# Kernel optimization log

Hardware: AMD Instinct MI355X
Metric: run time of the kernel (lower is better)

The kernel has to match this reference:

```python
import jax, jax.numpy as jnp
import numpy as np

N, IN, OUT, FAN = 4096, 4096, 4096, 64


def setup_inputs() -> dict:
    key = jax.random.key(0)
    k1, k2, k3, k4 = jax.random.split(key, 4)
    return {
        "input": jax.random.normal(k1, (N, IN), dtype=jnp.float32),
        "condensed_weight": jax.random.normal(k2, (OUT, FAN), dtype=jnp.float32) * np.float32(1.0 / np.sqrt(FAN)),
        "input_mask": jax.random.randint(k3, (OUT, FAN), 0, IN, dtype=jnp.int32),
        "bias": jax.random.normal(k4, (OUT,), dtype=jnp.float32),
    }


def reference(input, condensed_weight, input_mask, bias):
    # Fixed-fan-in sparse linear: out[b, o] = sum_k input[b, mask[o, k]] * W[o, k] + bias[o]
    # Scan over the (small, fixed) fan-in axis to avoid materializing the
    # [N, OUT, FAN] gathered tensor; each step gathers an [N, OUT] slab.
    n = input.shape[0]

    def body(acc, wk_mk):
        w_k, m_k = wk_mk            # each [OUT]
        g = jnp.take(input, m_k, axis=1)  # [N, OUT] gather of input columns
        return acc + g * w_k[None, :], None

    acc0 = jnp.zeros((n, bias.shape[0]), dtype=input.dtype) + bias[None, :]
    out, _ = jax.lax.scan(body, acc0, (condensed_weight.T, input_mask.T))
    return out
```

## Files before the change

### kernel.cpp

```cpp
#include <hip/hip_runtime.h>

#define IN_DIM   4096
#define OUT_DIM  4096
#define FAN_IN   64
#define ROWS     8
#define NTHREADS 512
#define O_PER_THREAD (OUT_DIM / NTHREADS)
#define MT_BYTES ((size_t)(FAN_IN / 4) * OUT_DIM * 16)

typedef __fp16 v2h __attribute__((ext_vector_type(2)));

__device__ __forceinline__ int bswz(int m) {
    return (m & ~7) | ((m ^ (m >> 3)) & 7);
}

__device__ __forceinline__ unsigned int pack_f16(float a, float b) {
    v2h h = __builtin_amdgcn_cvt_pkrtz(a, b);
    unsigned int u;
    __builtin_memcpy(&u, &h, sizeof(u));
    return u;
}

__global__ __launch_bounds__(256)
void transpose_mw(const int* __restrict__ M, const float* __restrict__ W,
                  int4* __restrict__ Mt, float4* __restrict__ Wt)
{
    const int t  = blockIdx.x * 256 + threadIdx.x;
    const int kk = t >> 12;
    const int o  = t & (OUT_DIM - 1);
    int4 m = ((const int4*)(M + (size_t)o * FAN_IN))[kk];
    m.x = bswz(m.x) << 4; m.y = bswz(m.y) << 4;
    m.z = bswz(m.z) << 4; m.w = bswz(m.w) << 4;
    Mt[kk * OUT_DIM + o] = m;
    Wt[kk * OUT_DIM + o] = ((const float4*)(W + (size_t)o * FAN_IN))[kk];
}

#define FMAMIX_LO(acc, pk, w)                                                  \
    asm("v_fma_mix_f32 %0, %1, %2, %0 op_sel:[0,0,0] op_sel_hi:[1,0,0]"        \
        : "+v"(acc) : "v"(pk), "v"(w))
#define FMAMIX_HI(acc, pk, w)                                                  \
    asm("v_fma_mix_f32 %0, %1, %2, %0 op_sel:[1,0,0] op_sel_hi:[1,0,0]"        \
        : "+v"(acc) : "v"(pk), "v"(w))

template <bool TRANSPOSED>
__global__ __launch_bounds__(NTHREADS, 4)
void ffi_sparse_kernel(const float* __restrict__ inp,
                       const float* __restrict__ W,
                       const int*   __restrict__ M,
                       const float* __restrict__ bias,
                       const int4*  __restrict__ Mt,
                       const float4* __restrict__ Wt,
                       float* __restrict__ out)
{
    __shared__ unsigned int lds[IN_DIM * ROWS / 2];

    const int tid = threadIdx.x;
    const int r0  = blockIdx.x * ROWS;

    #pragma unroll
    for (int t = 0; t < (ROWS * IN_DIM / 16) / NTHREADS; ++t) {
        const int tile = tid + t * NTHREADS;
        const int rblk = tile >> 10;
        const int c4   = (tile & 1023) << 2;
        const float* src = inp + (size_t)(r0 + rblk * 4) * IN_DIM + c4;
        const float4 v0 = *(const float4*)(src);
        const float4 v1 = *(const float4*)(src + IN_DIM);
        const float4 v2 = *(const float4*)(src + 2 * IN_DIM);
        const float4 v3 = *(const float4*)(src + 3 * IN_DIM);

        unsigned int* p;
        p = lds + bswz(c4 + 0) * 4 + rblk * 2;
        *(uint2*)p = make_uint2(pack_f16(v0.x, v1.x), pack_f16(v2.x, v3.x));
        p = lds + bswz(c4 + 1) * 4 + rblk * 2;
        *(uint2*)p = make_uint2(pack_f16(v0.y, v1.y), pack_f16(v2.y, v3.y));
        p = lds + bswz(c4 + 2) * 4 + rblk * 2;
        *(uint2*)p = make_uint2(pack_f16(v0.z, v1.z), pack_f16(v2.z, v3.z));
        p = lds + bswz(c4 + 3) * 4 + rblk * 2;
        *(uint2*)p = make_uint2(pack_f16(v0.w, v1.w), pack_f16(v2.w, v3.w));
    }
    __syncthreads();

    const char* __restrict__ ldsb = (const char*)lds;

#define LDQ(off) (*(const uint4*)(ldsb + (off)))

#define CONSUME(d, wv) {                                                       \
        FMAMIX_LO(acc0, d.x, wv);  FMAMIX_HI(acc1, d.x, wv);                   \
        FMAMIX_LO(acc2, d.y, wv);  FMAMIX_HI(acc3, d.y, wv);                   \
        FMAMIX_LO(acc4, d.z, wv);  FMAMIX_HI(acc5, d.z, wv);                   \
        FMAMIX_LO(acc6, d.w, wv);  FMAMIX_HI(acc7, d.w, wv);                   \
    }
#define ISSUE4(D0,D1,D2,D3, MN) {                                              \
        D0 = LDQ(MN.x); D1 = LDQ(MN.y); D2 = LDQ(MN.z); D3 = LDQ(MN.w); }
#define CONS4(D0,D1,D2,D3, WC) {                                               \
        CONSUME(D0, WC.x); CONSUME(D1, WC.y);                                  \
        CONSUME(D2, WC.z); CONSUME(D3, WC.w); }
#define MWLD(dm, dw, idx) {                                                    \
        if (TRANSPOSED) {                                                      \
            dm = Mt[(idx) * OUT_DIM + o];                                      \
            dw = Wt[(idx) * OUT_DIM + o];                                      \
        } else {                                                               \
            int4 mr = mp[(idx)];                                               \
            mr.x = bswz(mr.x) << 4; mr.y = bswz(mr.y) << 4;                    \
            mr.z = bswz(mr.z) << 4; mr.w = bswz(mr.w) << 4;                    \
            dm = mr; dw = wp[(idx)];                                           \
        } }

    #pragma unroll 1
    for (int i = 0; i < O_PER_THREAD; ++i) {
        const int o = tid + i * NTHREADS;
        const float bv = bias[o];
        float acc0 = bv, acc1 = bv, acc2 = bv, acc3 = bv;
        float acc4 = bv, acc5 = bv, acc6 = bv, acc7 = bv;

        const int4*   mp = (const int4*)(M + (size_t)o * FAN_IN);
        const float4* wp = (const float4*)(W + (size_t)o * FAN_IN);

        int4   m0, m1, m2, m3;
        float4 w0, w1, w2, w3;
        uint4  dA0, dA1, dA2, dA3, dB0, dB1, dB2, dB3;

        MWLD(m0, w0, 0);  MWLD(m1, w1, 1);  MWLD(m2, w2, 2);
        ISSUE4(dA0,dA1,dA2,dA3, m0);

        ISSUE4(dB0,dB1,dB2,dB3, m1);  MWLD(m3,w3, 3);   CONS4(dA0,dA1,dA2,dA3, w0);
        ISSUE4(dA0,dA1,dA2,dA3, m2);  MWLD(m0,w0, 4);   CONS4(dB0,dB1,dB2,dB3, w1);
        ISSUE4(dB0,dB1,dB2,dB3, m3);  MWLD(m1,w1, 5);   CONS4(dA0,dA1,dA2,dA3, w2);
        ISSUE4(dA0,dA1,dA2,dA3, m0);  MWLD(m2,w2, 6);   CONS4(dB0,dB1,dB2,dB3, w3);
        ISSUE4(dB0,dB1,dB2,dB3, m1);  MWLD(m3,w3, 7);   CONS4(dA0,dA1,dA2,dA3, w0);
        ISSUE4(dA0,dA1,dA2,dA3, m2);  MWLD(m0,w0, 8);   CONS4(dB0,dB1,dB2,dB3, w1);
        ISSUE4(dB0,dB1,dB2,dB3, m3);  MWLD(m1,w1, 9);   CONS4(dA0,dA1,dA2,dA3, w2);
        ISSUE4(dA0,dA1,dA2,dA3, m0);  MWLD(m2,w2,10);   CONS4(dB0,dB1,dB2,dB3, w3);
        ISSUE4(dB0,dB1,dB2,dB3, m1);  MWLD(m3,w3,11);   CONS4(dA0,dA1,dA2,dA3, w0);
        ISSUE4(dA0,dA1,dA2,dA3, m2);  MWLD(m0,w0,12);   CONS4(dB0,dB1,dB2,dB3, w1);
        ISSUE4(dB0,dB1,dB2,dB3, m3);  MWLD(m1,w1,13);   CONS4(dA0,dA1,dA2,dA3, w2);
        ISSUE4(dA0,dA1,dA2,dA3, m0);  MWLD(m2,w2,14);   CONS4(dB0,dB1,dB2,dB3, w3);
        ISSUE4(dB0,dB1,dB2,dB3, m1);  MWLD(m3,w3,15);   CONS4(dA0,dA1,dA2,dA3, w0);
        ISSUE4(dA0,dA1,dA2,dA3, m2);                    CONS4(dB0,dB1,dB2,dB3, w1);
        ISSUE4(dB0,dB1,dB2,dB3, m3);                    CONS4(dA0,dA1,dA2,dA3, w2);
                                                        CONS4(dB0,dB1,dB2,dB3, w3);

        float* op = out + (size_t)r0 * OUT_DIM + o;
        op[0 * OUT_DIM] = acc0;
        op[1 * OUT_DIM] = acc1;
        op[2 * OUT_DIM] = acc2;
        op[3 * OUT_DIM] = acc3;
        op[4 * OUT_DIM] = acc4;
        op[5 * OUT_DIM] = acc5;
        op[6 * OUT_DIM] = acc6;
        op[7 * OUT_DIM] = acc7;
    }
#undef CONSUME
#undef ISSUE4
#undef CONS4
#undef MWLD
#undef LDQ
}

extern "C" void kernel_launch(void* const* d_in, const int* in_sizes, int n_in,
                              void* d_out, int out_size, void* d_ws, size_t ws_size,
                              hipStream_t stream) {
    const float* inp  = (const float*)d_in[0];
    const float* W    = (const float*)d_in[1];
    const int*   M    = (const int*)d_in[2];
    const float* bias = (const float*)d_in[3];
    float* out = (float*)d_out;

    const int n_rows = in_sizes[0] / IN_DIM;
    dim3 grid(n_rows / ROWS), block(NTHREADS);

    const bool use_t = ws_size >= 2 * MT_BYTES;
    if (use_t) {
        int4*   Mt = (int4*)d_ws;
        float4* Wt = (float4*)((char*)d_ws + MT_BYTES);
        transpose_mw<<<dim3(OUT_DIM * (FAN_IN / 4) / 256), dim3(256), 0, stream>>>(M, W, Mt, Wt);
        ffi_sparse_kernel<true><<<grid, block, 0, stream>>>(inp, W, M, bias, Mt, Wt, out);
    } else {
        ffi_sparse_kernel<false><<<grid, block, 0, stream>>>(inp, W, M, bias,
                                                             (const int4*)nullptr,
                                                             (const float4*)nullptr, out);
    }
}
```

Before: 74.55 us.

## Reorder fan-in indices per output to spread LDS bank groups across lanes

The preprocessing kernel now handles one output per thread and reorders its 64 fan-in entries by LDS bank group. Each step s aims for group (s+o)&7, so neighbouring lanes read different bank groups at the same time, which is meant to cut LDS bank conflicts in the gather loop. The cost is that the setup kernel becomes serial per thread with large local arrays, likely spilling to scratch, and it launches only 16 blocks. That extra setup time adds to the total.

Result: slower. 133.1 us (+78.5%).

```diff
diff --git a/kernel.cpp b/kernel.cpp
--- a/kernel.cpp
+++ b/kernel.cpp
@@ -22,17 +22,47 @@
 }
 
 __global__ __launch_bounds__(256)
-void transpose_mw(const int* __restrict__ M, const float* __restrict__ W,
-                  int4* __restrict__ Mt, float4* __restrict__ Wt)
+void schedule_mw(const int* __restrict__ M, const float* __restrict__ W,
+                 int4* __restrict__ Mt, float4* __restrict__ Wt)
 {
-    const int t  = blockIdx.x * 256 + threadIdx.x;
-    const int kk = t >> 12;
-    const int o  = t & (OUT_DIM - 1);
-    int4 m = ((const int4*)(M + (size_t)o * FAN_IN))[kk];
-    m.x = bswz(m.x) << 4; m.y = bswz(m.y) << 4;
-    m.z = bswz(m.z) << 4; m.w = bswz(m.w) << 4;
-    Mt[kk * OUT_DIM + o] = m;
-    Wt[kk * OUT_DIM + o] = ((const float4*)(W + (size_t)o * FAN_IN))[kk];
+    const int o = blockIdx.x * 256 + threadIdx.x;
+
+    int   mm[FAN_IN];
+    float ww[FAN_IN];
+    int   gg[FAN_IN];
+    for (int k = 0; k < FAN_IN; ++k) {
+        const int m = M[(size_t)o * FAN_IN + k];
+        mm[k] = bswz(m) << 4;
+        gg[k] = (mm[k] >> 4) & 7;
+        ww[k] = W[(size_t)o * FAN_IN + k];
+    }
+    int cnt[8] = {0,0,0,0,0,0,0,0};
+    for (int k = 0; k < FAN_IN; ++k) cnt[gg[k]]++;
+    int start[8]; int acc0 = 0;
+    for (int g = 0; g < 8; ++g) { start[g] = acc0; acc0 += cnt[g]; }
+    int fill[8] = {0,0,0,0,0,0,0,0};
+    int order[FAN_IN];
+    for (int k = 0; k < FAN_IN; ++k) order[start[gg[k]] + fill[gg[k]]++] = k;
+    int ptr[8] = {0,0,0,0,0,0,0,0};
+    int4 tm; float4 tw;
+    for (int s = 0; s < FAN_IN; ++s) {
+        int d = (s + o) & 7;
+        if (ptr[d] >= cnt[d]) {
+            int best = 0, bestrem = -1;
+            for (int g = 0; g < 8; ++g) {
+                const int rem = cnt[g] - ptr[g];
+                if (rem > bestrem) { bestrem = rem; best = g; }
+            }
+            d = best;
+        }
+        const int k = order[start[d] + ptr[d]++];
+        ((int*)&tm)[s & 3]   = mm[k];
+        ((float*)&tw)[s & 3] = ww[k];
+        if ((s & 3) == 3) {
+            Mt[(s >> 2) * OUT_DIM + o] = tm;
+            Wt[(s >> 2) * OUT_DIM + o] = tw;
+        }
+    }
 }
 
 #define FMAMIX_LO(acc, pk, w)                                                  \
@@ -173,7 +203,7 @@
     if (use_t) {
         int4*   Mt = (int4*)d_ws;
         float4* Wt = (float4*)((char*)d_ws + MT_BYTES);
-        transpose_mw<<<dim3(OUT_DIM * (FAN_IN / 4) / 256), dim3(256), 0, stream>>>(M, W, Mt, Wt);
+        schedule_mw<<<dim3(OUT_DIM / 256), dim3(256), 0, stream>>>(M, W, Mt, Wt);
         ffi_sparse_kernel<true><<<grid, block, 0, stream>>>(inp, W, M, bias, Mt, Wt, out);
     } else {
         ffi_sparse_kernel<false><<<grid, block, 0, stream>>>(inp, W, M, bias,
```

## Reorder per-output fan-in indices to spread LDS gathers across banks

Applied to the files above, without the earlier changes.

The preprocessing kernel now permutes each output's 64 (index, weight) pairs instead of only transposing them. Each pair is assigned to a slot by its LDS bank group and rotated by the output index, so the 16-byte gathers issued together by neighbouring threads fall into different bank groups. Overflow entries from crowded groups fill the gaps left by sparse ones. This targets LDS bank conflicts in the main gather-FMA loop, at the cost of a more complex ballot/popcount scheduling pass, and it relies on the sum being order-independent.

Measured after the change: 71.99 us. 3.4% less time.

```diff
diff --git a/kernel.cpp b/kernel.cpp
--- a/kernel.cpp
+++ b/kernel.cpp
@@ -22,17 +22,50 @@
 }
 
 __global__ __launch_bounds__(256)
-void transpose_mw(const int* __restrict__ M, const float* __restrict__ W,
-                  int4* __restrict__ Mt, float4* __restrict__ Wt)
+void schedule_mw(const int* __restrict__ M, const float* __restrict__ W,
+                 int* __restrict__ Mt, float* __restrict__ Wt)
 {
-    const int t  = blockIdx.x * 256 + threadIdx.x;
-    const int kk = t >> 12;
-    const int o  = t & (OUT_DIM - 1);
-    int4 m = ((const int4*)(M + (size_t)o * FAN_IN))[kk];
-    m.x = bswz(m.x) << 4; m.y = bswz(m.y) << 4;
-    m.z = bswz(m.z) << 4; m.w = bswz(m.w) << 4;
-    Mt[kk * OUT_DIM + o] = m;
-    Wt[kk * OUT_DIM + o] = ((const float4*)(W + (size_t)o * FAN_IN))[kk];
+    const int o = blockIdx.x * 4 + (threadIdx.x >> 6);
+    const int k = threadIdx.x & 63;
+
+    const int   m    = M[(size_t)o * FAN_IN + k];
+    const float w    = W[(size_t)o * FAN_IN + k];
+    const int   moff = bswz(m) << 4;
+    const int   g    = (moff >> 4) & 7;
+
+    int cnt[8];
+    unsigned long long same = 0;
+    #pragma unroll
+    for (int h = 0; h < 8; ++h) {
+        const unsigned long long b = __ballot(g == h);
+        cnt[h] = __popcll(b);
+        if (g == h) same = b;
+    }
+    const unsigned long long ltmask = (k == 0) ? 0ULL : (~0ULL >> (64 - k));
+    const int r = __popcll(same & ltmask);
+
+    int slot;
+    if (r < 8) {
+        slot = ((g - o) & 7) + 8 * r;
+    } else {
+        int ovr = r - 8;
+        #pragma unroll
+        for (int h = 0; h < 8; ++h)
+            if (h < g && cnt[h] > 8) ovr += cnt[h] - 8;
+        int hstar = 0, jstar = 0, rem = ovr;
+        bool found = false;
+        #pragma unroll
+        for (int h = 0; h < 8; ++h) {
+            const int nh = (cnt[h] < 8) ? (8 - cnt[h]) : 0;
+            if (!found && rem < nh) { hstar = h; jstar = cnt[h] + rem; found = true; }
+            if (!found) rem -= nh;
+        }
+        slot = ((hstar - o) & 7) + 8 * jstar;
+    }
+
+    const int idx = ((slot >> 2) * OUT_DIM + o) * 4 + (slot & 3);
+    Mt[idx] = moff;
+    Wt[idx] = w;
 }
 
 #define FMAMIX_LO(acc, pk, w)                                                  \
@@ -171,10 +204,12 @@
 
     const bool use_t = ws_size >= 2 * MT_BYTES;
     if (use_t) {
-        int4*   Mt = (int4*)d_ws;
-        float4* Wt = (float4*)((char*)d_ws + MT_BYTES);
-        transpose_mw<<<dim3(OUT_DIM * (FAN_IN / 4) / 256), dim3(256), 0, stream>>>(M, W, Mt, Wt);
-        ffi_sparse_kernel<true><<<grid, block, 0, stream>>>(inp, W, M, bias, Mt, Wt, out);
+        int*   Mt = (int*)d_ws;
+        float* Wt = (float*)((char*)d_ws + MT_BYTES);
+        schedule_mw<<<dim3(OUT_DIM / 4), dim3(256), 0, stream>>>(M, W, Mt, Wt);
+        ffi_sparse_kernel<true><<<grid, block, 0, stream>>>(inp, W, M, bias,
+                                                            (const int4*)Mt,
+                                                            (const float4*)Wt, out);
     } else {
         ffi_sparse_kernel<false><<<grid, block, 0, stream>>>(inp, W, M, bias,
                                                              (const int4*)nullptr,
```
